# Kernel optimization log

Hardware: AMD Instinct MI355X
Metric: run time of the kernel (lower is better)

Reference implementation:

```python
import jax, jax.numpy as jnp
import numpy as np

B, T, D = 32, 1024, 384
T_OUT = 4096  # static padded output length (= target_len for every batch element)


def setup_inputs() -> dict:
    key = jax.random.key(0)
    k1, k2 = jax.random.split(key)
    x = jax.random.normal(k1, (B, T, D), dtype=jnp.float32)
    durations = jax.random.randint(k2, (B, T), 0, 8, dtype=jnp.int32)
    # constant target length -> torch pads/truncates every row to T_OUT,
    # and max over batch is T_OUT, so output is [B, T_OUT, D].
    target_len = jnp.full((B,), T_OUT, dtype=jnp.int32)
    return {"x": x, "durations": durations, "target_len": target_len}


def reference(x, durations, target_len):
    # x: [B, T, D]; durations: [B, T] int; target_len: [B] int.
    # Ragged repeat-expansion expressed as cumulative-duration searchsorted + gather.
    Bx, Tx, Dx = x.shape
    dur = jnp.maximum(durations, 0)
    ends = jnp.cumsum(dur, axis=1)              # [B, T] exclusive-end frame index per token
    total = ends[:, -1]                          # [B] total expanded length per batch row
    pos = jnp.arange(T_OUT, dtype=ends.dtype)    # [T_OUT] output frame positions
    # token index owning each output frame: number of ends <= pos
    idx = jax.vmap(lambda e: jnp.searchsorted(e, pos, side="right"))(ends)  # [B, T_OUT]
    idx = jnp.clip(idx, 0, Tx - 1)
    out = jnp.take_along_axis(x, idx[..., None], axis=1)  # [B, T_OUT, D]
    # frames past min(total_expansion, target_len) are zero padding (truncate + pad semantics)
    limit = jnp.minimum(total, target_len.astype(total.dtype))  # [B]
    valid = pos[None, :] < limit[:, None]                        # [B, T_OUT]
    return jnp.where(valid[..., None], out, jnp.zeros((), x.dtype))
```

## Files before the change

### kernel.cpp

```cpp
#include <hip/hip_runtime.h>


#define BB 32
#define TT 1024
#define TOUT 4096
#define D4 96
#define N4 (TOUT * D4)
#define EPB 3072
#define ROWS_PB 32
#define KPT 12

typedef float v4f __attribute__((ext_vector_type(4)));

__global__ __launch_bounds__(256) void lr_fused(
    const int4* __restrict__ dur4,
    const int* __restrict__ target_len,
    const v4f* __restrict__ x,
    v4f* __restrict__ out)
{
    __shared__ int s_ends[TT];
    __shared__ int s_wsum[4];
    __shared__ int s_trow[ROWS_PB];
    const int b = blockIdx.y;
    const int tid = threadIdx.x;
    const int lane = tid & 63;
    const int wave = tid >> 6;
    const int base0 = blockIdx.x * EPB;
    const int p0 = blockIdx.x * ROWS_PB;

    const int tl = target_len[b];

    int4 d = dur4[b * 256 + tid];
    const int d0 = d.x > 0 ? d.x : 0;
    const int d1 = d.y > 0 ? d.y : 0;
    const int d2 = d.z > 0 ? d.z : 0;
    const int d3 = d.w > 0 ? d.w : 0;
    const int e0 = d0, e1 = e0 + d1, e2 = e1 + d2, e3 = e2 + d3;

    int v = e3;
    #pragma unroll
    for (int off = 1; off < 64; off <<= 1) {
        int u = __shfl_up(v, off, 64);
        if (lane >= off) v += u;
    }
    if (lane == 63) s_wsum[wave] = v;
    __syncthreads();

    int wbase = 0;
    #pragma unroll
    for (int w = 0; w < 3; ++w) wbase += (w < wave) ? s_wsum[w] : 0;
    const int total = s_wsum[0] + s_wsum[1] + s_wsum[2] + s_wsum[3];
    const int lim = total < tl ? total : tl;

    const int base = wbase + v - e3;
    ((int4*)s_ends)[tid] = make_int4(base + e0, base + e1, base + e2, base + e3);
    __syncthreads();

    if (tid < ROWS_PB) {
        const int p = p0 + tid;
        int lo = 0;
        #pragma unroll
        for (int s = 512; s > 0; s >>= 1) {
            lo += (s_ends[lo + s - 1] <= p) ? s : 0;
        }
        s_trow[tid] = lo;
    }
    __syncthreads();

    const v4f* __restrict__ x_b = x + b * TT * D4;
    v4f* __restrict__ out_b = out + b * N4;

    int pp[KPT], cc[KPT], tt[KPT];
    v4f vv[KPT];
    #pragma unroll
    for (int k = 0; k < KPT; ++k) {
        const int i = base0 + k * 256 + tid;
        const int p = i / D4;
        pp[k] = p;
        cc[k] = i - p * D4;
        tt[k] = s_trow[p - p0];
    }
    #pragma unroll
    for (int k = 0; k < KPT; ++k) {
        vv[k] = x_b[tt[k] * D4 + cc[k]];
    }
    #pragma unroll
    for (int k = 0; k < KPT; ++k) {
        if (pp[k] >= lim) vv[k] = (v4f)(0.f);
        __builtin_nontemporal_store(vv[k], out_b + base0 + k * 256 + tid);
    }
}

extern "C" void kernel_launch(void* const* d_in, const int* in_sizes, int n_in,
                              void* d_out, int out_size, void* d_ws, size_t ws_size,
                              hipStream_t stream) {
    const float* x        = (const float*)d_in[0];
    const int* durations  = (const int*)d_in[1];
    const int* target_len = (const int*)d_in[2];
    float* out            = (float*)d_out;

    dim3 grid(N4 / EPB, BB);
    lr_fused<<<grid, 256, 0, stream>>>((const int4*)durations, target_len,
                                       (const v4f*)x, (v4f*)out);
}
```

Measured before the change: 241.3 us.

## Split index computation into separate kernel and skip loads for padded frames

```diff
diff --git a/kernel.cpp b/kernel.cpp
--- a/kernel.cpp
+++ b/kernel.cpp
@@ -9,8 +9,103 @@
 #define EPB 3072
 #define ROWS_PB 32
 #define KPT 12
+#define IDX_GROUPS 4
 
 typedef float v4f __attribute__((ext_vector_type(4)));
+
+__global__ __launch_bounds__(256) void lr_index(
+    const int4* __restrict__ dur4,
+    const int* __restrict__ target_len,
+    short* __restrict__ t_idx)
+{
+    __shared__ int s_ends[TT];
+    __shared__ int s_wsum[4];
+    const int b = blockIdx.x;
+    const int g = blockIdx.y;
+    const int tid = threadIdx.x;
+    const int lane = tid & 63;
+    const int wave = tid >> 6;
+    const int tl = target_len[b];
+
+    int4 d = dur4[b * 256 + tid];
+    const int d0 = d.x > 0 ? d.x : 0;
+    const int d1 = d.y > 0 ? d.y : 0;
+    const int d2 = d.z > 0 ? d.z : 0;
+    const int d3 = d.w > 0 ? d.w : 0;
+    const int e0 = d0, e1 = e0 + d1, e2 = e1 + d2, e3 = e2 + d3;
+
+    int v = e3;
+    #pragma unroll
+    for (int off = 1; off < 64; off <<= 1) {
+        int u = __shfl_up(v, off, 64);
+        if (lane >= off) v += u;
+    }
+    if (lane == 63) s_wsum[wave] = v;
+    __syncthreads();
+
+    int wbase = 0;
+    #pragma unroll
+    for (int w = 0; w < 3; ++w) wbase += (w < wave) ? s_wsum[w] : 0;
+    const int total = s_wsum[0] + s_wsum[1] + s_wsum[2] + s_wsum[3];
+    const int lim = total < tl ? total : tl;
+
+    const int base = wbase + v - e3;
+    ((int4*)s_ends)[tid] = make_int4(base + e0, base + e1, base + e2, base + e3);
+    __syncthreads();
+
+    short* __restrict__ trow_b = t_idx + b * TOUT;
+    #pragma unroll
+    for (int k = 0; k < 4; ++k) {
+        const int p = g * 1024 + k * 256 + tid;
+        int lo = 0;
+        #pragma unroll
+        for (int s = 512; s > 0; s >>= 1) {
+            lo += (s_ends[lo + s - 1] <= p) ? s : 0;
+        }
+        trow_b[p] = (p < lim) ? (short)lo : (short)-1;
+    }
+}
+
+__global__ __launch_bounds__(256) void lr_gather(
+    const short* __restrict__ t_idx,
+    const v4f* __restrict__ x,
+    v4f* __restrict__ out)
+{
+    __shared__ short s_trow[ROWS_PB];
+    const int b = blockIdx.y;
+    const int tid = threadIdx.x;
+    const int base0 = blockIdx.x * EPB;
+    const int p0 = blockIdx.x * ROWS_PB;
+
+    if (tid < ROWS_PB) s_trow[tid] = t_idx[b * TOUT + p0 + tid];
+    __syncthreads();
+
+    const v4f* __restrict__ x_b = x + b * TT * D4;
+    v4f* __restrict__ out_b = out + b * N4;
+
+    int tt[KPT], cc[KPT];
+    #pragma unroll
+    for (int k = 0; k < KPT; ++k) {
+        const int i = base0 + k * 256 + tid;
+        const int p = i / D4;
+        cc[k] = i - p * D4;
+        tt[k] = s_trow[p - p0];
+    }
+
+    v4f vv[KPT];
+    #pragma unroll
+    for (int k = 0; k < KPT; ++k) {
+        v4f val = (v4f)(0.f);
+        const int t = tt[k];
+        if (t >= 0) val = x_b[t * D4 + cc[k]];
+        vv[k] = val;
+    }
+
+    #pragma unroll
+    for (int k = 0; k < KPT; ++k) {
+        __builtin_nontemporal_store(vv[k], out_b + base0 + k * 256 + tid);
+    }
+}
 
 __global__ __launch_bounds__(256) void lr_fused(
     const int4* __restrict__ dur4,
@@ -70,19 +165,19 @@
     const v4f* __restrict__ x_b = x + b * TT * D4;
     v4f* __restrict__ out_b = out + b * N4;
 
-    int pp[KPT], cc[KPT], tt[KPT];
+    int pp[KPT], ccc[KPT], ttt[KPT];
     v4f vv[KPT];
     #pragma unroll
     for (int k = 0; k < KPT; ++k) {
         const int i = base0 + k * 256 + tid;
         const int p = i / D4;
         pp[k] = p;
-        cc[k] = i - p * D4;
-        tt[k] = s_trow[p - p0];
-    }
-    #pragma unroll
-    for (int k = 0; k < KPT; ++k) {
-        vv[k] = x_b[tt[k] * D4 + cc[k]];
+        ccc[k] = i - p * D4;
+        ttt[k] = s_trow[p - p0];
+    }
+    #pragma unroll
+    for (int k = 0; k < KPT; ++k) {
+        vv[k] = x_b[ttt[k] * D4 + ccc[k]];
     }
     #pragma unroll
     for (int k = 0; k < KPT; ++k) {
@@ -99,7 +194,15 @@
     const int* target_len = (const int*)d_in[2];
     float* out            = (float*)d_out;
 
-    dim3 grid(N4 / EPB, BB);
-    lr_fused<<<grid, 256, 0, stream>>>((const int4*)durations, target_len,
-                                       (const v4f*)x, (v4f*)out);
-}
+    const size_t need = (size_t)BB * TOUT * sizeof(short);
+    if (d_ws != nullptr && ws_size >= need) {
+        short* t_idx = (short*)d_ws;
+        lr_index<<<dim3(BB, IDX_GROUPS), 256, 0, stream>>>(
+            (const int4*)durations, target_len, t_idx);
+        lr_gather<<<dim3(N4 / EPB, BB), 256, 0, stream>>>(
+            t_idx, (const v4f*)x, (v4f*)out);
+    } else {
+        lr_fused<<<dim3(N4 / EPB, BB), 256, 0, stream>>>(
+            (const int4*)durations, target_len, (const v4f*)x, (v4f*)out);
+    }
+}
```

After: 245.9 us. Within noise of the previous version (+1.9%).
